# Kernel tuning notes

Measured on AMD Instinct MI355X. Metric: run time of the kernel, lower is better.

The kernel has to match this reference:

```python
import jax, jax.numpy as jnp
import numpy as np

B, S, D, H, O, E, K = 8, 2048, 768, 3072, 768, 8, 2
LN_EPS = 1e-5


def setup_inputs() -> dict:
    key = jax.random.key(0)
    ks = jax.random.split(key, 8)
    x = jax.random.normal(ks[0], (B, S, D), dtype=jnp.float32)
    router_w = jax.random.normal(ks[1], (D, E), dtype=jnp.float32) * 0.02
    router_b = jnp.zeros((E,), dtype=jnp.float32)
    w1 = jax.random.normal(ks[2], (E, D, H), dtype=jnp.float32) * 0.02
    b1 = jnp.zeros((E, H), dtype=jnp.float32)
    w2 = jax.random.normal(ks[3], (E, H, O), dtype=jnp.float32) * 0.02
    b2 = jnp.zeros((E, O), dtype=jnp.float32)
    ln_g = jnp.ones((O,), dtype=jnp.float32)
    ln_b = jnp.zeros((O,), dtype=jnp.float32)
    return {"x": x, "router_w": router_w, "router_b": router_b,
            "w1": w1, "b1": b1, "w2": w2, "b2": b2,
            "ln_g": ln_g, "ln_b": ln_b}


def _layernorm(y, g, b):
    mu = jnp.mean(y, axis=-1, keepdims=True)
    var = jnp.mean(jnp.square(y - mu), axis=-1, keepdims=True)
    return (y - mu) * jax.lax.rsqrt(var + LN_EPS) * g + b


def reference(x, router_w, router_b, w1, b1, w2, b2, ln_g, ln_b):
    # Router (NoisyTopKRouter, eval mode: no noise): top-k gate over expert logits
    logits = jnp.einsum('bsd,de->bse', x, router_w) + router_b   # [B,S,E]
    top_vals, top_idx = jax.lax.top_k(logits, K)                 # [B,S,K]
    routing_weights = jax.nn.softmax(top_vals, axis=-1)          # [B,S,K]

    out = jnp.zeros((B, S, O), dtype=x.dtype)
    for e in range(E):
        # per-token combined weight for this expert (0 if not routed)
        w_e = jnp.sum(routing_weights * (top_idx == e), axis=-1)  # [B,S]
        # dense per-expert feedforward on ALL tokens (as in original loop)
        h = jax.nn.gelu(jnp.einsum('bsd,dh->bsh', x, w1[e]) + b1[e])
        y = jnp.einsum('bsh,ho->bso', h, w2[e]) + b2[e]
        out = out + y * w_e[..., None]
    return _layernorm(out, ln_g, ln_b)
```

## Files before the change

kernel.cpp:

```cpp
#include <hip/hip_runtime.h>
#include <hip/hip_bf16.h>
#include <stdint.h>

#define Bq  8
#define Sq  2048
#define Dq  768
#define Hq  3072
#define Oq  768
#define Eq  8
#define Mq  (Bq*Sq)
#define LN_EPS 1e-5f
#define MAX_T256 (Mq/128 + 16)

typedef unsigned short u16;
typedef __attribute__((ext_vector_type(4))) float f32x4;
typedef __attribute__((ext_vector_type(8))) __bf16 bf16x8;

static __device__ __forceinline__ u16 f2bf(float f) {
  __hip_bfloat16 h = __float2bfloat16(f);
  return __builtin_bit_cast(u16, h);
}

static __device__ __forceinline__ float gelu_f(float x) {
  float u = 0.7978845608028654f * x * (1.0f + 0.044715f * x * x);
  float e = __expf(2.0f * u);
  float t = 1.0f - 2.0f / (e + 1.0f);
  return 0.5f * x * (1.0f + t);
}

typedef const __attribute__((address_space(1))) void* gas_t;
typedef __attribute__((address_space(3))) void* las_t;
static __device__ __forceinline__ void gload16(const void* g, void* l) {
  __builtin_amdgcn_global_load_lds((gas_t)g, (las_t)l, 16, 0, 0);
}

__global__ __launch_bounds__(256) void router_cvt_kernel(
    const float* __restrict__ x, const float* __restrict__ rw,
    const float* __restrict__ rb, u16* __restrict__ Xbf,
    int* __restrict__ tok_seg, float2* __restrict__ tok_w,
    int* __restrict__ cnt)
{
  if (blockIdx.x == 0 && threadIdx.x < 16) cnt[threadIdx.x] = 0;

  __shared__ float rwT[Eq * Dq];
  for (int i = threadIdx.x; i < Eq * Dq; i += 256)
    rwT[(i & 7) * Dq + (i >> 3)] = rw[i];
  __syncthreads();

  int wid = threadIdx.x >> 6;
  int lane = threadIdx.x & 63;
  int token = blockIdx.x * 4 + wid;
  const float4* xrow = (const float4*)(x + (size_t)token * Dq);
  ushort4* orow = (ushort4*)(Xbf + (size_t)token * Dq);

  float acc[Eq];
#pragma unroll
  for (int e = 0; e < Eq; e++) acc[e] = 0.f;

#pragma unroll
  for (int it = 0; it < Dq / 256; it++) {
    int d4 = it * 64 + lane;
    float4 xv = xrow[d4];
    ushort4 o;
    o.x = f2bf(xv.x); o.y = f2bf(xv.y); o.z = f2bf(xv.z); o.w = f2bf(xv.w);
    orow[d4] = o;
    int d = d4 * 4;
#pragma unroll
    for (int e = 0; e < Eq; e++) {
      float4 wv = *(const float4*)&rwT[e * Dq + d];
      acc[e] += xv.x * wv.x + xv.y * wv.y + xv.z * wv.z + xv.w * wv.w;
    }
  }
#pragma unroll
  for (int e = 0; e < Eq; e++) {
    float v = acc[e];
#pragma unroll
    for (int off = 32; off; off >>= 1) v += __shfl_xor(v, off);
    acc[e] = v;
  }
  if (lane == 0) {
    float v1 = -1e30f, v2 = -1e30f; int i1 = 0, i2 = 0;
#pragma unroll
    for (int e = 0; e < Eq; e++) {
      float v = acc[e] + rb[e];
      if (v > v1)      { v2 = v1; i2 = i1; v1 = v; i1 = e; }
      else if (v > v2) { v2 = v;  i2 = e; }
    }
    float ex = expf(v2 - v1);
    float wa = 1.f / (1.f + ex);
    float wb = ex / (1.f + ex);
    tok_seg[token] = i1 | ((8 + i2) << 8);
    tok_w[token] = make_float2(wa, wb);
  }
}

__global__ __launch_bounds__(256) void scatter_build(
    const int* __restrict__ tok_seg, const float2* __restrict__ tok_w,
    int* __restrict__ cnt, int* __restrict__ seg_tok, float* __restrict__ seg_wgt)
{
  __shared__ int histA[16], histB[16], base[16];
  int t = threadIdx.x;
  if (t < 16) { histA[t] = 0; histB[t] = 0; }
  __syncthreads();
  int token = blockIdx.x * 256 + t;
  int sp = tok_seg[token];
  float2 wv = tok_w[token];
  int s0 = sp & 0xff, s1 = sp >> 8;
  atomicAdd(&histA[s0], 1);
  atomicAdd(&histA[s1], 1);
  __syncthreads();
  if (t < 16) base[t] = atomicAdd(&cnt[t], histA[t]);
  __syncthreads();
  int p0 = base[s0] + atomicAdd(&histB[s0], 1);
  seg_tok[(size_t)s0 * Mq + p0] = token;
  seg_wgt[(size_t)s0 * Mq + p0] = wv.x;
  int p1 = base[s1] + atomicAdd(&histB[s1], 1);
  seg_tok[(size_t)s1 * Mq + p1] = token;
  seg_wgt[(size_t)s1 * Mq + p1] = wv.y;
}

__global__ __launch_bounds__(256) void transpose_cvt2(
    const float* __restrict__ w1, u16* __restrict__ W1T,
    const float* __restrict__ w2, u16* __restrict__ W2T)
{
  __shared__ float tile[32][33];
  const int which = blockIdx.z;
  const int R = which ? Hq : Dq;
  const int C = which ? Oq : Hq;
  const int NC = C / 32;
  const float* in = (which ? w2 : w1) + (size_t)blockIdx.y * R * C;
  u16* out = (which ? W2T : W1T) + (size_t)blockIdx.y * R * C;
  const int idx = blockIdx.x;
  const int c0 = (idx % NC) * 32, r0 = (idx / NC) * 32;
  int tx = threadIdx.x & 31, ty = threadIdx.x >> 5;
#pragma unroll
  for (int rr = 0; rr < 32; rr += 8)
    tile[rr + ty][tx] = in[(size_t)(r0 + rr + ty) * C + c0 + tx];
  __syncthreads();
#pragma unroll
  for (int rr = 0; rr < 32; rr += 8)
    out[(size_t)(c0 + rr + ty) * R + r0 + tx] = f2bf(tile[tx][rr + ty]);
}

__global__ __launch_bounds__(512, 2) void moe_gemm1(
    const u16* __restrict__ A, const u16* __restrict__ W,
    const float* __restrict__ bias, u16* __restrict__ Hout,
    const int* __restrict__ cnt, const int* __restrict__ seg_tok,
    int K, int N, int tile_lo)
{
  const int NP = N / 256;
  const int lid = (int)blockIdx.x + NP * (int)blockIdx.y;
  const int xcd = lid & 7, slot = lid >> 3;
  const int t_loc = xcd + 8 * (slot / NP);
  const int panel = slot % NP;

  const int t = tile_lo + t_loc;
  int pfx[16];
  {
    int tot = 0;
#pragma unroll
    for (int s2 = 0; s2 < 16; s2++) { pfx[s2] = tot; tot += (cnt[s2] + 255) >> 8; }
    if (t >= tot) return;
  }
  int seg = 0;
#pragma unroll
  for (int s2 = 1; s2 < 16; s2++) if (pfx[s2] <= t) seg = s2;
  const int e = seg & 7;
  const int segcnt = cnt[seg];
  const int ti = t - pfx[seg];
  const int lt = t_loc;

  __shared__ u16 smem[65536];
  const int tid  = threadIdx.x;
  const int lane = tid & 63;
  const int wid  = tid >> 6;
  const int wr   = wid >> 2, wc = wid & 3;
  const int lrow = lane & 15, kgrp = lane >> 4;
  const int gcx0 = ((kgrp)     ^ (lrow & 7)) * 8;
  const int gcx1 = ((4 + kgrp) ^ (lrow & 7)) * 8;

  f32x4 acc[8][4];
#pragma unroll
  for (int m = 0; m < 8; m++)
#pragma unroll
    for (int n = 0; n < 4; n++) acc[m][n] = (f32x4){0.f, 0.f, 0.f, 0.f};

  const int srow = tid >> 3;
  const int swz  = ((tid & 7) ^ (srow & 7)) * 8;
  const u16 *pA00, *pA01, *pA10, *pA11, *pB00, *pB01, *pB10, *pB11;
  {
    int sr;
    sr = ti * 256 +   0 +  0 + srow;
    pA00 = A + (size_t)((sr < segcnt) ? seg_tok[(size_t)seg * Mq + sr] : 0) * K + swz;
    sr = ti * 256 +   0 + 64 + srow;
    pA01 = A + (size_t)((sr < segcnt) ? seg_tok[(size_t)seg * Mq + sr] : 0) * K + swz;
    sr = ti * 256 + 128 +  0 + srow;
    pA10 = A + (size_t)((sr < segcnt) ? seg_tok[(size_t)seg * Mq + sr] : 0) * K + swz;
    sr = ti * 256 + 128 + 64 + srow;
    pA11 = A + (size_t)((sr < segcnt) ? seg_tok[(size_t)seg * Mq + sr] : 0) * K + swz;
    const u16* Wb = W + (size_t)e * K * N;
    pB00 = Wb + (size_t)(panel * 256 +   0 +  0 + srow) * K + swz;
    pB01 = Wb + (size_t)(panel * 256 +   0 + 64 + srow) * K + swz;
    pB10 = Wb + (size_t)(panel * 256 + 128 +  0 + srow) * K + swz;
    pB11 = Wb + (size_t)(panel * 256 + 128 + 64 + srow) * K + swz;
  }

#define STG(base, h, P0, P1)                               \
  do {                                                     \
    gload16(P0, &smem[(base) + (h) * 8192 + tid * 8]);     \
    gload16(P1, &smem[(base) + (h) * 8192 + 4096 + tid * 8]); \
    P0 += 64; P1 += 64;                                    \
  } while (0)

  const int NKT = K / 64;
  STG(0, 0, pA00, pA01); STG(0, 1, pA10, pA11);
  STG(32768, 0, pB00, pB01); STG(32768, 1, pB10, pB11);

  bf16x8 bfr[4][2];
  for (int kt = 0; kt < NKT; ++kt) {
    const int s = kt & 1;
    const int sA = s * 16384, sB = 32768 + s * 16384;
    const int dA = (s ^ 1) * 16384, dB = 32768 + (s ^ 1) * 16384;
    const bool more = (kt + 1 < NKT);
    const int abase = wr * 128 + lrow;
    const int bbase = wc * 64 + lrow;

    if (more) {
      STG(dA, 0, pA00, pA01);
      asm volatile("s_waitcnt vmcnt(2)" ::: "memory");
    } else {
      asm volatile("s_waitcnt vmcnt(0)" ::: "memory");
    }
    __builtin_amdgcn_s_barrier();
    __builtin_amdgcn_sched_barrier(0);
#pragma unroll
    for (int n = 0; n < 4; n++) {
      bfr[n][0] = *(const bf16x8*)&smem[sB + (bbase + n * 16) * 64 + gcx0];
      bfr[n][1] = *(const bf16x8*)&smem[sB + (bbase + n * 16) * 64 + gcx1];
    }
    {
      bf16x8 a00 = *(const bf16x8*)&smem[sA + (abase +  0) * 64 + gcx0];
      bf16x8 a01 = *(const bf16x8*)&smem[sA + (abase +  0) * 64 + gcx1];
      bf16x8 a10 = *(const bf16x8*)&smem[sA + (abase + 16) * 64 + gcx0];
      bf16x8 a11 = *(const bf16x8*)&smem[sA + (abase + 16) * 64 + gcx1];
      __builtin_amdgcn_s_setprio(1);
#pragma unroll
      for (int n = 0; n < 4; n++) {
        acc[0][n] = __builtin_amdgcn_mfma_f32_16x16x32_bf16(a00, bfr[n][0], acc[0][n], 0, 0, 0);
        acc[0][n] = __builtin_amdgcn_mfma_f32_16x16x32_bf16(a01, bfr[n][1], acc[0][n], 0, 0, 0);
        acc[1][n] = __builtin_amdgcn_mfma_f32_16x16x32_bf16(a10, bfr[n][0], acc[1][n], 0, 0, 0);
        acc[1][n] = __builtin_amdgcn_mfma_f32_16x16x32_bf16(a11, bfr[n][1], acc[1][n], 0, 0, 0);
      }
      __builtin_amdgcn_s_setprio(0);
    }
    __builtin_amdgcn_sched_barrier(0);
    __builtin_amdgcn_s_barrier();

#define PHASE(q, STGSTMT)                                                     \
    do {                                                                      \
      bf16x8 a00 = *(const bf16x8*)&smem[sA + (abase + (2*(q))    * 16) * 64 + gcx0]; \
      bf16x8 a01 = *(const bf16x8*)&smem[sA + (abase + (2*(q))    * 16) * 64 + gcx1]; \
      bf16x8 a10 = *(const bf16x8*)&smem[sA + (abase + (2*(q)+1)  * 16) * 64 + gcx0]; \
      bf16x8 a11 = *(const bf16x8*)&smem[sA + (abase + (2*(q)+1)  * 16) * 64 + gcx1]; \
      if (more) { STGSTMT; }                                                  \
      __builtin_amdgcn_s_setprio(1);                                          \
      _Pragma("unroll")                                                       \
      for (int n = 0; n < 4; n++) {                                           \
        acc[2*(q)][n]   = __builtin_amdgcn_mfma_f32_16x16x32_bf16(a00, bfr[n][0], acc[2*(q)][n], 0, 0, 0);   \
        acc[2*(q)][n]   = __builtin_amdgcn_mfma_f32_16x16x32_bf16(a01, bfr[n][1], acc[2*(q)][n], 0, 0, 0);   \
        acc[2*(q)+1][n] = __builtin_amdgcn_mfma_f32_16x16x32_bf16(a10, bfr[n][0], acc[2*(q)+1][n], 0, 0, 0); \
        acc[2*(q)+1][n] = __builtin_amdgcn_mfma_f32_16x16x32_bf16(a11, bfr[n][1], acc[2*(q)+1][n], 0, 0, 0); \
      }                                                                       \
      __builtin_amdgcn_s_setprio(0);                                          \
      __builtin_amdgcn_sched_barrier(0);                                      \
      __builtin_amdgcn_s_barrier();                                           \
    } while (0)

    PHASE(1, STG(dA, 1, pA10, pA11));
    PHASE(2, STG(dB, 0, pB00, pB01));
    PHASE(3, STG(dB, 1, pB10, pB11));
#undef PHASE
  }
#undef STG

  {
    const int rb = wr * 128, cb = wc * 64;
#pragma unroll
    for (int n = 0; n < 4; n++) {
      int cc = cb + n * 16 + lrow;
      float bv = bias[(size_t)e * N + panel * 256 + cc];
#pragma unroll
      for (int m = 0; m < 8; m++)
#pragma unroll
        for (int j = 0; j < 4; j++) {
          int rr = rb + m * 16 + kgrp * 4 + j;
          smem[rr * 256 + cc] = f2bf(gelu_f(acc[m][n][j] + bv));
        }
    }
    __syncthreads();
    const int r = tid >> 5, c8 = (tid & 31) * 8;
    u16* gdst = Hout + (size_t)(lt * 256) * N + (size_t)panel * 256;
#pragma unroll
    for (int it2 = 0; it2 < 16; ++it2) {
      int rr = it2 * 16 + r;
      *(uint4*)(gdst + (size_t)rr * N + c8) = *(const uint4*)&smem[rr * 256 + c8];
    }
  }
}

__global__ __launch_bounds__(256) void moe_gemm2(
    const u16* __restrict__ A, const u16* __restrict__ W,
    const float* __restrict__ bias, float* __restrict__ out,
    const int* __restrict__ cnt, const int* __restrict__ seg_tok,
    const float* __restrict__ seg_wgt, int K, int N, int tile_lo)
{
  const int NP = N / 128;
  const int lid = (int)blockIdx.x + NP * (int)blockIdx.y;
  const int xcd = lid & 7, slot = lid >> 3;
  const int t2 = xcd + 8 * (slot / NP);
  const int panel = slot % NP;

  const int t256 = tile_lo + (t2 >> 1);
  int pfx[16];
  {
    int tot = 0;
#pragma unroll
    for (int s2 = 0; s2 < 16; s2++) { pfx[s2] = tot; tot += (cnt[s2] + 255) >> 8; }
    if (t256 >= tot) return;
  }
  int seg = 0;
#pragma unroll
  for (int s2 = 1; s2 < 16; s2++) if (pfx[s2] <= t256) seg = s2;
  const int e = seg & 7;
  const int segcnt = cnt[seg];
  const int ti = (t256 - pfx[seg]) * 2 + (t2 & 1);
  const int lt = t2;

  __shared__ u16 As[2][128 * 32];
  __shared__ u16 Bs[2][128 * 32];
  const int tid  = threadIdx.x;
  const int lane = tid & 63;
  const int wid  = tid >> 6;
  const int wr   = wid >> 1, wc = wid & 1;
  const int lrow = lane & 15, kgrp = lane >> 4;
  const int kx   = kgrp ^ ((lrow >> 1) & 3);
  const int n0 = panel * 128;

  f32x4 acc[4][4];
#pragma unroll
  for (int m = 0; m < 4; m++)
#pragma unroll
    for (int n = 0; n < 4; n++) acc[m][n] = (f32x4){0.f, 0.f, 0.f, 0.f};

  const int r0 = tid >> 2;
  const int kc = (((tid & 3) ^ ((tid >> 3) & 3)) * 8);
  const u16* gA0 = A + (size_t)(lt * 128 + r0) * K + kc;
  const u16* gA1 = gA0 + (size_t)64 * K;
  const u16* gB = W + (size_t)e * K * N + (size_t)(n0 + r0) * K + kc;
  const size_t rowskipB = (size_t)64 * K;
  const int lofs = tid * 8;

  auto stage = [&](int b) {
    gload16(gA0, &As[b][lofs]);
    gload16(gA1, &As[b][lofs + 2048]);
    gload16(gB,            &Bs[b][lofs]);
    gload16(gB + rowskipB, &Bs[b][lofs + 2048]);
    gA0 += 32; gA1 += 32; gB += 32;
  };

  const int NIT = K / 32;
  stage(0);
  for (int it = 0; it < NIT; ++it) {
    const int cur = it & 1;
    if (it + 1 < NIT) {
      stage(cur ^ 1);
      asm volatile("s_waitcnt vmcnt(4)" ::: "memory");
    } else {
      asm volatile("s_waitcnt vmcnt(0)" ::: "memory");
    }
    __builtin_amdgcn_s_barrier();
    __builtin_amdgcn_sched_barrier(0);
    bf16x8 a[4], b[4];
#pragma unroll
    for (int m = 0; m < 4; m++)
      a[m] = *(const bf16x8*)&As[cur][(wr * 64 + m * 16 + lrow) * 32 + kx * 8];
#pragma unroll
    for (int n = 0; n < 4; n++)
      b[n] = *(const bf16x8*)&Bs[cur][(wc * 64 + n * 16 + lrow) * 32 + kx * 8];
#pragma unroll
    for (int m = 0; m < 4; m++)
#pragma unroll
      for (int n = 0; n < 4; n++)
        acc[m][n] = __builtin_amdgcn_mfma_f32_16x16x32_bf16(a[m], b[n], acc[m][n], 0, 0, 0);
    __builtin_amdgcn_sched_barrier(0);
    __builtin_amdgcn_s_barrier();
  }

  const int rbase = wr * 64;
  const int cbase = n0 + wc * 64;
#pragma unroll
  for (int m = 0; m < 4; m++)
#pragma unroll
    for (int j = 0; j < 4; j++) {
      int r = rbase + m * 16 + kgrp * 4 + j;
      int i = ti * 128 + r;
      if (i < segcnt) {
        int token = seg_tok[(size_t)seg * Mq + i];
        float w = seg_wgt[(size_t)seg * Mq + i];
        float* orow = out + (size_t)token * Oq;
#pragma unroll
        for (int n = 0; n < 4; n++) {
          int c = cbase + n * 16 + lrow;
          float v = (acc[m][n][j] + bias[(size_t)e * N + c]) * w;
          unsafeAtomicAdd(&orow[c], v);
        }
      }
    }
}

__global__ __launch_bounds__(256) void ln_kernel(
    float* __restrict__ io, const float* __restrict__ g, const float* __restrict__ b)
{
  int wid = threadIdx.x >> 6, lane = threadIdx.x & 63;
  int row = blockIdx.x * 4 + wid;
  float4* p = (float4*)(io + (size_t)row * Oq);
  float4 v[3];
  float s = 0.f;
#pragma unroll
  for (int i = 0; i < 3; i++) {
    v[i] = p[lane + i * 64];
    s += v[i].x + v[i].y + v[i].z + v[i].w;
  }
#pragma unroll
  for (int off = 32; off; off >>= 1) s += __shfl_xor(s, off);
  float mu = s * (1.0f / Oq);
  float q = 0.f;
#pragma unroll
  for (int i = 0; i < 3; i++) {
    float d0 = v[i].x - mu, d1 = v[i].y - mu, d2 = v[i].z - mu, d3 = v[i].w - mu;
    q += d0 * d0 + d1 * d1 + d2 * d2 + d3 * d3;
  }
#pragma unroll
  for (int off = 32; off; off >>= 1) q += __shfl_xor(q, off);
  float inv = rsqrtf(q * (1.0f / Oq) + LN_EPS);
#pragma unroll
  for (int i = 0; i < 3; i++) {
    int c = (lane + i * 64) * 4;
    float4 gv = *(const float4*)(g + c);
    float4 bv = *(const float4*)(b + c);
    float4 o;
    o.x = (v[i].x - mu) * inv * gv.x + bv.x;
    o.y = (v[i].y - mu) * inv * gv.y + bv.y;
    o.z = (v[i].z - mu) * inv * gv.z + bv.z;
    o.w = (v[i].w - mu) * inv * gv.w + bv.w;
    p[lane + i * 64] = o;
  }
}

extern "C" void kernel_launch(void* const* d_in, const int* in_sizes, int n_in,
                              void* d_out, int out_size, void* d_ws, size_t ws_size,
                              hipStream_t stream)
{
  const float* x    = (const float*)d_in[0];
  const float* rw   = (const float*)d_in[1];
  const float* rb   = (const float*)d_in[2];
  const float* w1   = (const float*)d_in[3];
  const float* b1   = (const float*)d_in[4];
  const float* w2   = (const float*)d_in[5];
  const float* b2   = (const float*)d_in[6];
  const float* ln_g = (const float*)d_in[7];
  const float* ln_b = (const float*)d_in[8];
  float* out = (float*)d_out;

  char* ws = (char*)d_ws;
  size_t off = 0;
  auto alloc = [&](size_t bytes) {
    void* p = ws + off;
    off += (bytes + 255) & ~(size_t)255;
    return p;
  };
  int*    cnt     = (int*)alloc(16 * 4);
  int*    tok_seg = (int*)alloc((size_t)Mq * 4);
  float2* tok_w   = (float2*)alloc((size_t)Mq * 8);
  int*    seg_tok = (int*)alloc((size_t)16 * Mq * 4);
  float*  seg_wgt = (float*)alloc((size_t)16 * Mq * 4);
  u16* Xbf = (u16*)alloc((size_t)Mq * Dq * 2);
  u16* W1T = (u16*)alloc((size_t)Eq * Dq * Hq * 2);
  u16* W2T = (u16*)alloc((size_t)Eq * Hq * Oq * 2);

  size_t remain = (ws_size > off) ? ws_size - off : 0;
  size_t tile_bytes = (size_t)256 * Hq * 2;
  long long wt = (long long)(remain / tile_bytes);
  if (wt > MAX_T256) wt = MAX_T256;
  wt &= ~7LL;
  if (wt < 8) wt = 8;
  int WT = (int)wt;
  u16* Hbuf = (u16*)alloc((size_t)WT * tile_bytes);

  hipMemsetAsync(out, 0, (size_t)Mq * Oq * 4, stream);
  router_cvt_kernel<<<Mq / 4, 256, 0, stream>>>(x, rw, rb, Xbf, tok_seg, tok_w, cnt);
  scatter_build<<<Mq / 256, 256, 0, stream>>>(tok_seg, tok_w, cnt, seg_tok, seg_wgt);
  transpose_cvt2<<<dim3((Dq / 32) * (Hq / 32), Eq, 2), 256, 0, stream>>>(
      w1, W1T, w2, W2T);

  for (int tl = 0; tl < MAX_T256; tl += WT) {
    int gx = MAX_T256 - tl; if (gx > WT) gx = WT;
    moe_gemm1<<<dim3(Hq / 256, gx), 512, 0, stream>>>(
        Xbf, W1T, b1, Hbuf, cnt, seg_tok, Dq, Hq, tl);
    moe_gemm2<<<dim3(Oq / 128, 2 * gx), 256, 0, stream>>>(
        Hbuf, W2T, b2, out, cnt, seg_tok, seg_wgt, Hq, Oq, tl);
  }
  ln_kernel<<<Mq / 4, 256, 0, stream>>>(out, ln_g, ln_b);
}
```

Baseline: 729.6 us.

## Replace atomic scatter-add with bf16 Y buffer and gather-combine in layernorm

The second GEMM now writes weighted expert outputs as bf16 rows into a per-segment Y buffer through shared memory with coalesced stores, instead of float atomics into the output. Scatter records each token's segment position, and a new layernorm kernel gathers the token's two expert rows, sums them, and normalizes. This removes the output memset and the atomic read-modify-write traffic. In exchange it rounds the expert outputs to bf16 before the combine and adds an extra buffer read.

```diff
diff --git a/kernel.cpp b/kernel.cpp
--- a/kernel.cpp
+++ b/kernel.cpp
@@ -20,6 +20,10 @@
   __hip_bfloat16 h = __float2bfloat16(f);
   return __builtin_bit_cast(u16, h);
 }
+static __device__ __forceinline__ float bf2f(u16 h) {
+  uint32_t u = (uint32_t)h << 16;
+  return __builtin_bit_cast(float, u);
+}
 
 static __device__ __forceinline__ float gelu_f(float x) {
   float u = 0.7978845608028654f * x * (1.0f + 0.044715f * x * x);
@@ -96,7 +100,8 @@
 
 __global__ __launch_bounds__(256) void scatter_build(
     const int* __restrict__ tok_seg, const float2* __restrict__ tok_w,
-    int* __restrict__ cnt, int* __restrict__ seg_tok, float* __restrict__ seg_wgt)
+    int* __restrict__ cnt, int* __restrict__ seg_tok, float* __restrict__ seg_wgt,
+    int2* __restrict__ tok_pos)
 {
   __shared__ int histA[16], histB[16], base[16];
   int t = threadIdx.x;
@@ -117,6 +122,7 @@
   int p1 = base[s1] + atomicAdd(&histB[s1], 1);
   seg_tok[(size_t)s1 * Mq + p1] = token;
   seg_wgt[(size_t)s1 * Mq + p1] = wv.y;
+  tok_pos[token] = make_int2(s0 | (p0 << 4), s1 | (p1 << 4));
 }
 
 __global__ __launch_bounds__(256) void transpose_cvt2(
@@ -310,7 +316,7 @@
 
 __global__ __launch_bounds__(256) void moe_gemm2(
     const u16* __restrict__ A, const u16* __restrict__ W,
-    const float* __restrict__ bias, float* __restrict__ out,
+    const float* __restrict__ bias, u16* __restrict__ Ybuf,
     const int* __restrict__ cnt, const int* __restrict__ seg_tok,
     const float* __restrict__ seg_wgt, int K, int N, int tile_lo)
 {
@@ -336,8 +342,7 @@
   const int ti = (t256 - pfx[seg]) * 2 + (t2 & 1);
   const int lt = t2;
 
-  __shared__ u16 As[2][128 * 32];
-  __shared__ u16 Bs[2][128 * 32];
+  __shared__ u16 smem[16384];
   const int tid  = threadIdx.x;
   const int lane = tid & 63;
   const int wid  = tid >> 6;
@@ -361,10 +366,10 @@
   const int lofs = tid * 8;
 
   auto stage = [&](int b) {
-    gload16(gA0, &As[b][lofs]);
-    gload16(gA1, &As[b][lofs + 2048]);
-    gload16(gB,            &Bs[b][lofs]);
-    gload16(gB + rowskipB, &Bs[b][lofs + 2048]);
+    gload16(gA0, &smem[b * 4096 + lofs]);
+    gload16(gA1, &smem[b * 4096 + lofs + 2048]);
+    gload16(gB,            &smem[8192 + b * 4096 + lofs]);
+    gload16(gB + rowskipB, &smem[8192 + b * 4096 + lofs + 2048]);
     gA0 += 32; gA1 += 32; gB += 32;
   };
 
@@ -383,10 +388,10 @@
     bf16x8 a[4], b[4];
 #pragma unroll
     for (int m = 0; m < 4; m++)
-      a[m] = *(const bf16x8*)&As[cur][(wr * 64 + m * 16 + lrow) * 32 + kx * 8];
+      a[m] = *(const bf16x8*)&smem[cur * 4096 + (wr * 64 + m * 16 + lrow) * 32 + kx * 8];
 #pragma unroll
     for (int n = 0; n < 4; n++)
-      b[n] = *(const bf16x8*)&Bs[cur][(wc * 64 + n * 16 + lrow) * 32 + kx * 8];
+      b[n] = *(const bf16x8*)&smem[8192 + cur * 4096 + (wc * 64 + n * 16 + lrow) * 32 + kx * 8];
 #pragma unroll
     for (int m = 0; m < 4; m++)
 #pragma unroll
@@ -396,64 +401,114 @@
     __builtin_amdgcn_s_barrier();
   }
 
-  const int rbase = wr * 64;
-  const int cbase = n0 + wc * 64;
-#pragma unroll
-  for (int m = 0; m < 4; m++)
-#pragma unroll
-    for (int j = 0; j < 4; j++) {
-      int r = rbase + m * 16 + kgrp * 4 + j;
-      int i = ti * 128 + r;
-      if (i < segcnt) {
-        int token = seg_tok[(size_t)seg * Mq + i];
-        float w = seg_wgt[(size_t)seg * Mq + i];
-        float* orow = out + (size_t)token * Oq;
+  {
+    const int rbase = wr * 64;
+    const int cbase = wc * 64;
+    float bv[4];
+#pragma unroll
+    for (int n = 0; n < 4; n++)
+      bv[n] = bias[(size_t)e * N + n0 + cbase + n * 16 + lrow];
+#pragma unroll
+    for (int m = 0; m < 4; m++)
+#pragma unroll
+      for (int j = 0; j < 4; j++) {
+        int r = rbase + m * 16 + kgrp * 4 + j;
+        int i = ti * 128 + r;
+        float w = (i < segcnt) ? seg_wgt[(size_t)seg * Mq + i] : 0.f;
 #pragma unroll
         for (int n = 0; n < 4; n++) {
           int c = cbase + n * 16 + lrow;
-          float v = (acc[m][n][j] + bias[(size_t)e * N + c]) * w;
-          unsafeAtomicAdd(&orow[c], v);
+          smem[r * 128 + c] = f2bf((acc[m][n][j] + bv[n]) * w);
         }
       }
-    }
-}
-
-__global__ __launch_bounds__(256) void ln_kernel(
-    float* __restrict__ io, const float* __restrict__ g, const float* __restrict__ b)
+    __syncthreads();
+    const size_t gi0 = (size_t)t256 * 256 + (size_t)(t2 & 1) * 128;
+    const int r = tid >> 4, c8 = (tid & 15) * 8;
+    u16* gdst = Ybuf + gi0 * Oq + n0;
+#pragma unroll
+    for (int p = 0; p < 8; ++p) {
+      int rr = p * 16 + r;
+      *(uint4*)(gdst + (size_t)rr * Oq + c8) = *(const uint4*)&smem[rr * 128 + c8];
+    }
+  }
+}
+
+__global__ __launch_bounds__(256) void ln2_kernel(
+    const u16* __restrict__ Ybuf, const int* __restrict__ cnt,
+    const int2* __restrict__ tok_pos, const float* __restrict__ g,
+    const float* __restrict__ b, float* __restrict__ out)
 {
   int wid = threadIdx.x >> 6, lane = threadIdx.x & 63;
-  int row = blockIdx.x * 4 + wid;
-  float4* p = (float4*)(io + (size_t)row * Oq);
-  float4 v[3];
+  int token = blockIdx.x * 4 + wid;
+  int pfx[16];
+  {
+    int tot = 0;
+#pragma unroll
+    for (int s = 0; s < 16; s++) { pfx[s] = tot; tot += (cnt[s] + 255) >> 8; }
+  }
+  int2 pp = tok_pos[token];
+  size_t gi0 = (size_t)pfx[pp.x & 15] * 256 + (pp.x >> 4);
+  size_t gi1 = (size_t)pfx[pp.y & 15] * 256 + (pp.y >> 4);
+  const u16* r0 = Ybuf + gi0 * Oq;
+  const u16* r1 = Ybuf + gi1 * Oq;
+
+  float v[12];
+  {
+    uint4 w0 = *(const uint4*)(r0 + lane * 8);
+    uint4 w1 = *(const uint4*)(r1 + lane * 8);
+    uint32_t u0[4] = {w0.x, w0.y, w0.z, w0.w};
+    uint32_t u1[4] = {w1.x, w1.y, w1.z, w1.w};
+#pragma unroll
+    for (int k = 0; k < 4; k++) {
+      v[2 * k]     = bf2f((u16)(u0[k] & 0xffff)) + bf2f((u16)(u1[k] & 0xffff));
+      v[2 * k + 1] = bf2f((u16)(u0[k] >> 16))    + bf2f((u16)(u1[k] >> 16));
+    }
+    ushort4 t0 = *(const ushort4*)(r0 + 512 + lane * 4);
+    ushort4 t1 = *(const ushort4*)(r1 + 512 + lane * 4);
+    v[8]  = bf2f(t0.x) + bf2f(t1.x);
+    v[9]  = bf2f(t0.y) + bf2f(t1.y);
+    v[10] = bf2f(t0.z) + bf2f(t1.z);
+    v[11] = bf2f(t0.w) + bf2f(t1.w);
+  }
+
   float s = 0.f;
 #pragma unroll
-  for (int i = 0; i < 3; i++) {
-    v[i] = p[lane + i * 64];
-    s += v[i].x + v[i].y + v[i].z + v[i].w;
-  }
+  for (int i = 0; i < 12; i++) s += v[i];
 #pragma unroll
   for (int off = 32; off; off >>= 1) s += __shfl_xor(s, off);
   float mu = s * (1.0f / Oq);
   float q = 0.f;
 #pragma unroll
-  for (int i = 0; i < 3; i++) {
-    float d0 = v[i].x - mu, d1 = v[i].y - mu, d2 = v[i].z - mu, d3 = v[i].w - mu;
-    q += d0 * d0 + d1 * d1 + d2 * d2 + d3 * d3;
-  }
+  for (int i = 0; i < 12; i++) { float d = v[i] - mu; q += d * d; }
 #pragma unroll
   for (int off = 32; off; off >>= 1) q += __shfl_xor(q, off);
   float inv = rsqrtf(q * (1.0f / Oq) + LN_EPS);
-#pragma unroll
-  for (int i = 0; i < 3; i++) {
-    int c = (lane + i * 64) * 4;
-    float4 gv = *(const float4*)(g + c);
-    float4 bv = *(const float4*)(b + c);
-    float4 o;
-    o.x = (v[i].x - mu) * inv * gv.x + bv.x;
-    o.y = (v[i].y - mu) * inv * gv.y + bv.y;
-    o.z = (v[i].z - mu) * inv * gv.z + bv.z;
-    o.w = (v[i].w - mu) * inv * gv.w + bv.w;
-    p[lane + i * 64] = o;
+
+  float* orow = out + (size_t)token * Oq;
+  {
+    float4 g0 = *(const float4*)(g + lane * 8);
+    float4 g1 = *(const float4*)(g + lane * 8 + 4);
+    float4 b0 = *(const float4*)(b + lane * 8);
+    float4 b1 = *(const float4*)(b + lane * 8 + 4);
+    float4 o0, o1;
+    o0.x = (v[0] - mu) * inv * g0.x + b0.x;
+    o0.y = (v[1] - mu) * inv * g0.y + b0.y;
+    o0.z = (v[2] - mu) * inv * g0.z + b0.z;
+    o0.w = (v[3] - mu) * inv * g0.w + b0.w;
+    o1.x = (v[4] - mu) * inv * g1.x + b1.x;
+    o1.y = (v[5] - mu) * inv * g1.y + b1.y;
+    o1.z = (v[6] - mu) * inv * g1.z + b1.z;
+    o1.w = (v[7] - mu) * inv * g1.w + b1.w;
+    *(float4*)(orow + lane * 8) = o0;
+    *(float4*)(orow + lane * 8 + 4) = o1;
+    float4 g2v = *(const float4*)(g + 512 + lane * 4);
+    float4 b2v = *(const float4*)(b + 512 + lane * 4);
+    float4 o2;
+    o2.x = (v[8]  - mu) * inv * g2v.x + b2v.x;
+    o2.y = (v[9]  - mu) * inv * g2v.y + b2v.y;
+    o2.z = (v[10] - mu) * inv * g2v.z + b2v.z;
+    o2.w = (v[11] - mu) * inv * g2v.w + b2v.w;
+    *(float4*)(orow + 512 + lane * 4) = o2;
   }
 }
 
@@ -482,11 +537,13 @@
   int*    cnt     = (int*)alloc(16 * 4);
   int*    tok_seg = (int*)alloc((size_t)Mq * 4);
   float2* tok_w   = (float2*)alloc((size_t)Mq * 8);
+  int2*   tok_pos = (int2*)alloc((size_t)Mq * 8);
   int*    seg_tok = (int*)alloc((size_t)16 * Mq * 4);
   float*  seg_wgt = (float*)alloc((size_t)16 * Mq * 4);
   u16* Xbf = (u16*)alloc((size_t)Mq * Dq * 2);
   u16* W1T = (u16*)alloc((size_t)Eq * Dq * Hq * 2);
   u16* W2T = (u16*)alloc((size_t)Eq * Hq * Oq * 2);
+  u16* Ybuf = (u16*)alloc((size_t)MAX_T256 * 256 * Oq * 2);
 
   size_t remain = (ws_size > off) ? ws_size - off : 0;
   size_t tile_bytes = (size_t)256 * Hq * 2;
@@ -497,9 +554,8 @@
   int WT = (int)wt;
   u16* Hbuf = (u16*)alloc((size_t)WT * tile_bytes);
 
-  hipMemsetAsync(out, 0, (size_t)Mq * Oq * 4, stream);
   router_cvt_kernel<<<Mq / 4, 256, 0, stream>>>(x, rw, rb, Xbf, tok_seg, tok_w, cnt);
-  scatter_build<<<Mq / 256, 256, 0, stream>>>(tok_seg, tok_w, cnt, seg_tok, seg_wgt);
+  scatter_build<<<Mq / 256, 256, 0, stream>>>(tok_seg, tok_w, cnt, seg_tok, seg_wgt, tok_pos);
   transpose_cvt2<<<dim3((Dq / 32) * (Hq / 32), Eq, 2), 256, 0, stream>>>(
       w1, W1T, w2, W2T);
 
@@ -508,7 +564,7 @@
     moe_gemm1<<<dim3(Hq / 256, gx), 512, 0, stream>>>(
         Xbf, W1T, b1, Hbuf, cnt, seg_tok, Dq, Hq, tl);
     moe_gemm2<<<dim3(Oq / 128, 2 * gx), 256, 0, stream>>>(
-        Hbuf, W2T, b2, out, cnt, seg_tok, seg_wgt, Hq, Oq, tl);
-  }
-  ln_kernel<<<Mq / 4, 256, 0, stream>>>(out, ln_g, ln_b);
-}
+        Hbuf, W2T, b2, Ybuf, cnt, seg_tok, seg_wgt, Hq, Oq, tl);
+  }
+  ln2_kernel<<<Mq / 4, 256, 0, stream>>>(Ybuf, cnt, tok_pos, ln_g, ln_b, out);
+}
```

After: 625.2 us. 14.3% less time.
